# Optimization experiments

Measured on AMD Instinct MI355X. Metric: run time of the kernel, lower is better.

Reference implementation:

```python
import jax, jax.numpy as jnp
import numpy as np

B, S, DIM = 32, 1, 4096
NH, NKV, HD = 32, 8, 128
N_REP = NH // NKV
MAX_SEQ = 2048
START_POS = 2047


def setup_inputs() -> dict:
    key = jax.random.key(0)
    ks = jax.random.split(key, 10)
    t = jnp.arange(S) + START_POS  # absolute positions of the new tokens
    inv_freq = 1.0 / (10000.0 ** (jnp.arange(0, HD, 2, dtype=jnp.float32) / HD))  # [HD/2]
    angles = t[:, None].astype(jnp.float32) * inv_freq[None, :]  # [S, HD/2]
    return {
        "x": jax.random.normal(ks[0], (B, S, DIM), dtype=jnp.float32),
        "freqs_cos": jnp.cos(angles),
        "freqs_sin": jnp.sin(angles),
        "cache_k": jax.random.normal(ks[1], (B, MAX_SEQ, NKV, HD), dtype=jnp.float32),
        "cache_v": jax.random.normal(ks[2], (B, MAX_SEQ, NKV, HD), dtype=jnp.float32),
        "wq": jax.random.normal(ks[3], (NH * HD, DIM), dtype=jnp.float32) * 0.02,
        "wk": jax.random.normal(ks[4], (NKV * HD, DIM), dtype=jnp.float32) * 0.02,
        "wv": jax.random.normal(ks[5], (NKV * HD, DIM), dtype=jnp.float32) * 0.02,
        "wo": jax.random.normal(ks[6], (NH * HD, DIM), dtype=jnp.float32).T * 0.02,  # stored [out,in]=[DIM, NH*HD]
        "start_pos": START_POS,
    }


def _apply_rope(t, cos, sin):
    # t: [B, S, H, HD]; cos/sin: [S, HD/2] -> broadcast [1, S, 1, HD/2]
    tr = t.reshape(*t.shape[:-1], HD // 2, 2)
    x0, x1 = tr[..., 0], tr[..., 1]
    c = cos[None, :, None, :]
    s = sin[None, :, None, :]
    o0 = x0 * c - x1 * s
    o1 = x0 * s + x1 * c
    return jnp.stack([o0, o1], axis=-1).reshape(t.shape)


def reference(x, freqs_cos, freqs_sin, cache_k, cache_v, wq, wk, wv, wo, start_pos):
    batch, seq_len, _ = x.shape
    xq = jnp.einsum('bsd,ed->bse', x, wq).reshape(batch, seq_len, NH, HD)
    xk = jnp.einsum('bsd,ed->bse', x, wk).reshape(batch, seq_len, NKV, HD)
    xv = jnp.einsum('bsd,ed->bse', x, wv).reshape(batch, seq_len, NKV, HD)

    xq = _apply_rope(xq, freqs_cos, freqs_sin)
    xk = _apply_rope(xk, freqs_cos, freqs_sin)

    # KV-cache scatter-write, then read prefix [0, start_pos+seq_len)
    ck = jax.lax.dynamic_update_slice(cache_k, xk, (0, start_pos, 0, 0))
    cv = jax.lax.dynamic_update_slice(cache_v, xv, (0, start_pos, 0, 0))
    T = start_pos + seq_len  # static Python int
    keys = ck[:, :T]    # [B, T, NKV, HD]
    values = cv[:, :T]  # [B, T, NKV, HD]

    # GQA without materializing repeat_kv: group query heads by kv head
    q = xq.reshape(batch, seq_len, NKV, N_REP, HD)
    scores = jnp.einsum('bsgrd,btgd->bgrst', q, keys) / jnp.sqrt(jnp.float32(HD))
    probs = jax.nn.softmax(scores.astype(jnp.float32), axis=-1).astype(xq.dtype)
    out = jnp.einsum('bgrst,btgd->bsgrd', probs, values)  # [B, S, NKV, N_REP, HD]
    out = out.reshape(batch, seq_len, NH * HD)
    return jnp.einsum('bse,de->bsd', out, wo)
```

## Files before the change

kernel.cpp:

```cpp
#include <hip/hip_runtime.h>
#include <hip/hip_bf16.h>

#define B     32
#define DIM   4096
#define NH    32
#define NKV   8
#define HD    128
#define TCACHE 2048
#define NREP  4
#define SPLIT 8
#define TS    256
#define CHUNK 256
#define NCH   (DIM / CHUNK)

__device__ __forceinline__ void gemm16_core(
    const float* __restrict__ inp, const float* __restrict__ W,
    float* __restrict__ outp, int stride, int row0, bool rope,
    const float* __restrict__ fc, const float* __restrict__ fs,
    float (*xs)[B][CHUNK])
{
    const int tid = threadIdx.x;
    const int rp  = tid >> 6;
    const int kt  = tid & 63;
    const int r0  = row0 + rp * 2;

    const float* w0 = W + (size_t)r0 * DIM;
    const float* w1 = w0 + DIM;

    const int sb = tid >> 4;
    const int sc = (tid << 4) & 255;
    const float* sbase = inp + (size_t)sb * DIM + sc;

    float acc0[B], acc1[B];
#pragma unroll
    for (int b = 0; b < B; ++b) { acc0[b] = 0.f; acc1[b] = 0.f; }

    float4 xr0 = *(const float4*)(sbase);
    float4 xr1 = *(const float4*)(sbase + 4);
    float4 xr2 = *(const float4*)(sbase + 8);
    float4 xr3 = *(const float4*)(sbase + 12);
    float4 wa0 = *(const float4*)(w0 + kt * 4);
    float4 wa1 = *(const float4*)(w1 + kt * 4);
    *(float4*)(&xs[0][sb][sc])      = xr0;
    *(float4*)(&xs[0][sb][sc + 4])  = xr1;
    *(float4*)(&xs[0][sb][sc + 8])  = xr2;
    *(float4*)(&xs[0][sb][sc + 12]) = xr3;

    int buf = 0;
    for (int ch = 0; ch < NCH; ++ch) {
        __syncthreads();
        float4 wb0, wb1;
        const bool more = (ch + 1 < NCH);
        if (more) {
            const int k1 = (ch + 1) * CHUNK;
            xr0 = *(const float4*)(sbase + k1);
            xr1 = *(const float4*)(sbase + k1 + 4);
            xr2 = *(const float4*)(sbase + k1 + 8);
            xr3 = *(const float4*)(sbase + k1 + 12);
            wb0 = *(const float4*)(w0 + k1 + kt * 4);
            wb1 = *(const float4*)(w1 + k1 + kt * 4);
        }
        const float* xrow = &xs[buf][0][kt * 4];
#pragma unroll
        for (int b = 0; b < B; ++b) {
            float4 xv = *(const float4*)(xrow + b * CHUNK);
            acc0[b] = fmaf(wa0.x, xv.x, acc0[b]);
            acc0[b] = fmaf(wa0.y, xv.y, acc0[b]);
            acc0[b] = fmaf(wa0.z, xv.z, acc0[b]);
            acc0[b] = fmaf(wa0.w, xv.w, acc0[b]);
            acc1[b] = fmaf(wa1.x, xv.x, acc1[b]);
            acc1[b] = fmaf(wa1.y, xv.y, acc1[b]);
            acc1[b] = fmaf(wa1.z, xv.z, acc1[b]);
            acc1[b] = fmaf(wa1.w, xv.w, acc1[b]);
        }
        if (more) {
            *(float4*)(&xs[buf ^ 1][sb][sc])      = xr0;
            *(float4*)(&xs[buf ^ 1][sb][sc + 4])  = xr1;
            *(float4*)(&xs[buf ^ 1][sb][sc + 8])  = xr2;
            *(float4*)(&xs[buf ^ 1][sb][sc + 12]) = xr3;
            wa0 = wb0; wa1 = wb1;
        }
        buf ^= 1;
    }

#pragma unroll
    for (int b = 0; b < B; ++b) {
        float v0 = acc0[b], v1 = acc1[b];
        for (int off = 1; off < 64; off <<= 1) {
            v0 += __shfl_xor(v0, off);
            v1 += __shfl_xor(v1, off);
        }
        acc0[b] = v0; acc1[b] = v1;
    }
    if (kt == 0) {
        float c = 1.f, s = 0.f;
        if (rope) { int i = (r0 & (HD - 1)) >> 1; c = fc[i]; s = fs[i]; }
#pragma unroll
        for (int b = 0; b < B; ++b) {
            float o0 = acc0[b], o1 = acc1[b];
            if (rope) { float t0 = o0 * c - o1 * s; o1 = o0 * s + o1 * c; o0 = t0; }
            outp[(size_t)b * stride + r0]     = o0;
            outp[(size_t)b * stride + r0 + 1] = o1;
        }
    }
}

__global__ __launch_bounds__(512) void qkv_gemm(
    const float* __restrict__ x,
    const float* __restrict__ wq, const float* __restrict__ wk, const float* __restrict__ wv,
    float* __restrict__ qo, float* __restrict__ ko, float* __restrict__ vo,
    const float* __restrict__ fc, const float* __restrict__ fs)
{
    __shared__ float xs[2][B][CHUNK];
    int blk = blockIdx.x;
    const float* W; float* outp; int stride, row0; bool rope;
    if (blk < 256)      { W = wq; outp = qo; stride = NH * HD;  row0 = blk * 16;         rope = true;  }
    else if (blk < 320) { W = wk; outp = ko; stride = NKV * HD; row0 = (blk - 256) * 16; rope = true;  }
    else                { W = wv; outp = vo; stride = NKV * HD; row0 = (blk - 320) * 16; rope = false; }
    gemm16_core(x, W, outp, stride, row0, rope, fc, fs, xs);
}

__global__ __launch_bounds__(512) void gemm_wo(
    const float* __restrict__ inp, const float* __restrict__ W, float* __restrict__ outp)
{
    __shared__ float xs[2][B][CHUNK];
    gemm16_core(inp, W, outp, DIM, blockIdx.x * 16, false, nullptr, nullptr, xs);
}

__global__ __launch_bounds__(256) void attn_split_k(
    const float* __restrict__ qr, const float* __restrict__ kn, const float* __restrict__ vn,
    const float* __restrict__ ck, const float* __restrict__ cv,
    float* __restrict__ part_o, float* __restrict__ part_ml)
{
    __shared__ float q_lds[NREP][HD];
    __shared__ float p_lds[TS][NREP];
    __shared__ float red[4][NREP];
    __shared__ float o_scr[8][NREP][HD];

    const int bid = blockIdx.x;
    const int s = bid & 7, h = (bid >> 3) & 7, b = bid >> 6;
    const int t0 = s * TS;
    const int tid = threadIdx.x;

    for (int i = tid; i < NREP * HD; i += 256)
        q_lds[i >> 7][i & 127] = qr[((size_t)b * NH + h * NREP + (i >> 7)) * HD + (i & 127)];
    __syncthreads();

    const int t = t0 + tid;
    const float* kptr = (t == TCACHE - 1)
        ? (kn + ((size_t)b * NKV + h) * HD)
        : (ck + (((size_t)b * TCACHE + t) * NKV + h) * HD);
    float s0 = 0.f, s1 = 0.f, s2 = 0.f, s3 = 0.f;
#pragma unroll 8
    for (int d = 0; d < HD; d += 4) {
        float4 kv = *(const float4*)(kptr + d);
        float4 q0 = *(const float4*)(&q_lds[0][d]);
        float4 q1 = *(const float4*)(&q_lds[1][d]);
        float4 q2 = *(const float4*)(&q_lds[2][d]);
        float4 q3 = *(const float4*)(&q_lds[3][d]);
        s0 = fmaf(q0.x, kv.x, s0); s0 = fmaf(q0.y, kv.y, s0); s0 = fmaf(q0.z, kv.z, s0); s0 = fmaf(q0.w, kv.w, s0);
        s1 = fmaf(q1.x, kv.x, s1); s1 = fmaf(q1.y, kv.y, s1); s1 = fmaf(q1.z, kv.z, s1); s1 = fmaf(q1.w, kv.w, s1);
        s2 = fmaf(q2.x, kv.x, s2); s2 = fmaf(q2.y, kv.y, s2); s2 = fmaf(q2.z, kv.z, s2); s2 = fmaf(q2.w, kv.w, s2);
        s3 = fmaf(q3.x, kv.x, s3); s3 = fmaf(q3.y, kv.y, s3); s3 = fmaf(q3.z, kv.z, s3); s3 = fmaf(q3.w, kv.w, s3);
    }
    const float scale = 0.088388347648318447f;
    s0 *= scale; s1 *= scale; s2 *= scale; s3 *= scale;

    float m0 = s0, m1 = s1, m2 = s2, m3 = s3;
    for (int off = 1; off < 64; off <<= 1) {
        m0 = fmaxf(m0, __shfl_xor(m0, off));
        m1 = fmaxf(m1, __shfl_xor(m1, off));
        m2 = fmaxf(m2, __shfl_xor(m2, off));
        m3 = fmaxf(m3, __shfl_xor(m3, off));
    }
    const int wv_ = tid >> 6, lane = tid & 63;
    if (lane == 0) { red[wv_][0] = m0; red[wv_][1] = m1; red[wv_][2] = m2; red[wv_][3] = m3; }
    __syncthreads();
    m0 = fmaxf(fmaxf(red[0][0], red[1][0]), fmaxf(red[2][0], red[3][0]));
    m1 = fmaxf(fmaxf(red[0][1], red[1][1]), fmaxf(red[2][1], red[3][1]));
    m2 = fmaxf(fmaxf(red[0][2], red[1][2]), fmaxf(red[2][2], red[3][2]));
    m3 = fmaxf(fmaxf(red[0][3], red[1][3]), fmaxf(red[2][3], red[3][3]));
    float p0 = __expf(s0 - m0), p1 = __expf(s1 - m1), p2 = __expf(s2 - m2), p3 = __expf(s3 - m3);
    *(float4*)(&p_lds[tid][0]) = make_float4(p0, p1, p2, p3);
    float l0 = p0, l1 = p1, l2 = p2, l3 = p3;
    for (int off = 1; off < 64; off <<= 1) {
        l0 += __shfl_xor(l0, off);
        l1 += __shfl_xor(l1, off);
        l2 += __shfl_xor(l2, off);
        l3 += __shfl_xor(l3, off);
    }
    __syncthreads();
    if (lane == 0) { red[wv_][0] = l0; red[wv_][1] = l1; red[wv_][2] = l2; red[wv_][3] = l3; }
    __syncthreads();
    if (tid < NREP) {
        float l = red[0][tid] + red[1][tid] + red[2][tid] + red[3][tid];
        float m = (tid == 0) ? m0 : (tid == 1) ? m1 : (tid == 2) ? m2 : m3;
        part_ml[(size_t)bid * 8 + tid * 2]     = m;
        part_ml[(size_t)bid * 8 + tid * 2 + 1] = l;
    }

    const int g  = tid >> 5;
    const int dl = (tid & 31) << 2;
    float4 a0 = make_float4(0,0,0,0), a1 = a0, a2 = a0, a3 = a0;
    const int tb = t0 + g * 32;
#pragma unroll 4
    for (int j = 0; j < 32; ++j) {
        int tt = tb + j;
        const float* vptr = (tt == TCACHE - 1)
            ? (vn + ((size_t)b * NKV + h) * HD)
            : (cv + (((size_t)b * TCACHE + tt) * NKV + h) * HD);
        float4 vvv = *(const float4*)(vptr + dl);
        float4 pp  = *(const float4*)(&p_lds[g * 32 + j][0]);
        a0.x = fmaf(pp.x, vvv.x, a0.x); a0.y = fmaf(pp.x, vvv.y, a0.y); a0.z = fmaf(pp.x, vvv.z, a0.z); a0.w = fmaf(pp.x, vvv.w, a0.w);
        a1.x = fmaf(pp.y, vvv.x, a1.x); a1.y = fmaf(pp.y, vvv.y, a1.y); a1.z = fmaf(pp.y, vvv.z, a1.z); a1.w = fmaf(pp.y, vvv.w, a1.w);
        a2.x = fmaf(pp.z, vvv.x, a2.x); a2.y = fmaf(pp.z, vvv.y, a2.y); a2.z = fmaf(pp.z, vvv.z, a2.z); a2.w = fmaf(pp.z, vvv.w, a2.w);
        a3.x = fmaf(pp.w, vvv.x, a3.x); a3.y = fmaf(pp.w, vvv.y, a3.y); a3.z = fmaf(pp.w, vvv.z, a3.z); a3.w = fmaf(pp.w, vvv.w, a3.w);
    }
    *(float4*)(&o_scr[g][0][dl]) = a0;
    *(float4*)(&o_scr[g][1][dl]) = a1;
    *(float4*)(&o_scr[g][2][dl]) = a2;
    *(float4*)(&o_scr[g][3][dl]) = a3;
    __syncthreads();
    for (int oi = tid; oi < NREP * HD; oi += 256) {
        int r = oi >> 7, d = oi & 127;
        float sum = 0.f;
#pragma unroll
        for (int gg = 0; gg < 8; ++gg) sum += o_scr[gg][r][d];
        part_o[((size_t)bid * NREP + r) * HD + d] = sum;
    }
}

__global__ __launch_bounds__(128) void attn_combine(
    const float* __restrict__ part_o, const float* __restrict__ part_ml,
    float* __restrict__ attn_out)
{
    const int bh = blockIdx.x;
    const int d  = threadIdx.x;
    const int b = bh >> 3, h = bh & 7;
#pragma unroll
    for (int r = 0; r < NREP; ++r) {
        float ms[SPLIT], ls[SPLIT];
        float M = -1e30f;
#pragma unroll
        for (int s = 0; s < SPLIT; ++s) {
            ms[s] = part_ml[(size_t)(bh * SPLIT + s) * 8 + r * 2];
            ls[s] = part_ml[(size_t)(bh * SPLIT + s) * 8 + r * 2 + 1];
            M = fmaxf(M, ms[s]);
        }
        float L = 0.f, o = 0.f;
#pragma unroll
        for (int s = 0; s < SPLIT; ++s) {
            float w = __expf(ms[s] - M);
            L += ls[s] * w;
            o = fmaf(w, part_o[((size_t)(bh * SPLIT + s) * NREP + r) * HD + d], o);
        }
        attn_out[((size_t)b * NH + (h * NREP + r)) * HD + d] = o / L;
    }
}

extern "C" void kernel_launch(void* const* d_in, const int* in_sizes, int n_in,
                              void* d_out, int out_size, void* d_ws, size_t ws_size,
                              hipStream_t stream)
{
    const float* x  = (const float*)d_in[0];
    const float* fc = (const float*)d_in[1];
    const float* fs = (const float*)d_in[2];
    const float* ck = (const float*)d_in[3];
    const float* cv = (const float*)d_in[4];
    const float* wq = (const float*)d_in[5];
    const float* wk = (const float*)d_in[6];
    const float* wv = (const float*)d_in[7];
    const float* wo = (const float*)d_in[8];

    float* ws   = (float*)d_ws;
    float* q_r  = ws;
    float* k_n  = ws + 131072;
    float* v_n  = ws + 163840;
    float* a_o  = ws + 196608;
    float* p_o  = ws + 327680;
    float* p_ml = ws + 1376256;
    float* outp = (float*)d_out;

    qkv_gemm<<<dim3(384), dim3(512), 0, stream>>>(x, wq, wk, wv, q_r, k_n, v_n, fc, fs);
    attn_split_k<<<dim3(B * NKV * SPLIT), dim3(256), 0, stream>>>(q_r, k_n, v_n, ck, cv, p_o, p_ml);
    attn_combine<<<dim3(B * NKV), dim3(128), 0, stream>>>(p_o, p_ml, a_o);
    gemm_wo<<<dim3(256), dim3(512), 0, stream>>>(a_o, wo, outp);
}
```

Baseline: 214.2 us.

## Coalesce attention K/V reads and split Wo GEMM over K with atomics

The attention kernel now reads K rows cooperatively: 32 lanes each load a float4 slice of one row, and the dot products are reduced with shuffles, replacing the per-thread strided row reads. V accumulation is changed to 64-lane float2 loads per row with 4 groups. Separately, the Wo GEMM is split into two K halves across 512 blocks, and the halves are summed with atomicAdd into an output that a new kernel zeroes first. This targets uncoalesced cache reads and low Wo-GEMM occupancy, at the cost of more shuffle work, atomics, an extra launch, and float summation order that is no longer deterministic.

After: 255.3 us. 19.2% more time.

```diff
diff --git a/kernel.cpp b/kernel.cpp
--- a/kernel.cpp
+++ b/kernel.cpp
@@ -11,25 +11,24 @@
 #define SPLIT 8
 #define TS    256
 #define CHUNK 256
-#define NCH   (DIM / CHUNK)
 
 __device__ __forceinline__ void gemm16_core(
     const float* __restrict__ inp, const float* __restrict__ W,
     float* __restrict__ outp, int stride, int row0, bool rope,
     const float* __restrict__ fc, const float* __restrict__ fs,
-    float (*xs)[B][CHUNK])
+    float (*xs)[B][CHUNK], int kbeg, int nch, bool atomic)
 {
     const int tid = threadIdx.x;
     const int rp  = tid >> 6;
     const int kt  = tid & 63;
     const int r0  = row0 + rp * 2;
 
-    const float* w0 = W + (size_t)r0 * DIM;
+    const float* w0 = W + (size_t)r0 * DIM + kbeg;
     const float* w1 = w0 + DIM;
 
     const int sb = tid >> 4;
     const int sc = (tid << 4) & 255;
-    const float* sbase = inp + (size_t)sb * DIM + sc;
+    const float* sbase = inp + (size_t)sb * DIM + kbeg + sc;
 
     float acc0[B], acc1[B];
 #pragma unroll
@@ -47,10 +46,10 @@
     *(float4*)(&xs[0][sb][sc + 12]) = xr3;
 
     int buf = 0;
-    for (int ch = 0; ch < NCH; ++ch) {
+    for (int ch = 0; ch < nch; ++ch) {
         __syncthreads();
         float4 wb0, wb1;
-        const bool more = (ch + 1 < NCH);
+        const bool more = (ch + 1 < nch);
         if (more) {
             const int k1 = (ch + 1) * CHUNK;
             xr0 = *(const float4*)(sbase + k1);
@@ -99,8 +98,13 @@
         for (int b = 0; b < B; ++b) {
             float o0 = acc0[b], o1 = acc1[b];
             if (rope) { float t0 = o0 * c - o1 * s; o1 = o0 * s + o1 * c; o0 = t0; }
-            outp[(size_t)b * stride + r0]     = o0;
-            outp[(size_t)b * stride + r0 + 1] = o1;
+            if (atomic) {
+                atomicAdd(&outp[(size_t)b * stride + r0],     o0);
+                atomicAdd(&outp[(size_t)b * stride + r0 + 1], o1);
+            } else {
+                outp[(size_t)b * stride + r0]     = o0;
+                outp[(size_t)b * stride + r0 + 1] = o1;
+            }
         }
     }
 }
@@ -117,14 +121,23 @@
     if (blk < 256)      { W = wq; outp = qo; stride = NH * HD;  row0 = blk * 16;         rope = true;  }
     else if (blk < 320) { W = wk; outp = ko; stride = NKV * HD; row0 = (blk - 256) * 16; rope = true;  }
     else                { W = wv; outp = vo; stride = NKV * HD; row0 = (blk - 320) * 16; rope = false; }
-    gemm16_core(x, W, outp, stride, row0, rope, fc, fs, xs);
-}
-
-__global__ __launch_bounds__(512) void gemm_wo(
+    gemm16_core(x, W, outp, stride, row0, rope, fc, fs, xs, 0, DIM / CHUNK, false);
+}
+
+__global__ __launch_bounds__(512) void gemm_wo_split(
     const float* __restrict__ inp, const float* __restrict__ W, float* __restrict__ outp)
 {
     __shared__ float xs[2][B][CHUNK];
-    gemm16_core(inp, W, outp, DIM, blockIdx.x * 16, false, nullptr, nullptr, xs);
+    const int rowblk = blockIdx.x >> 1;
+    const int kh     = blockIdx.x & 1;
+    gemm16_core(inp, W, outp, DIM, rowblk * 16, false, nullptr, nullptr, xs,
+                kh * (DIM / 2), (DIM / 2) / CHUNK, true);
+}
+
+__global__ __launch_bounds__(256) void zero_out_kernel(float4* __restrict__ p, int n4)
+{
+    int i = blockIdx.x * 256 + threadIdx.x;
+    if (i < n4) p[i] = make_float4(0.f, 0.f, 0.f, 0.f);
 }
 
 __global__ __launch_bounds__(256) void attn_split_k(
@@ -132,36 +145,64 @@
     const float* __restrict__ ck, const float* __restrict__ cv,
     float* __restrict__ part_o, float* __restrict__ part_ml)
 {
-    __shared__ float q_lds[NREP][HD];
     __shared__ float p_lds[TS][NREP];
     __shared__ float red[4][NREP];
-    __shared__ float o_scr[8][NREP][HD];
+    __shared__ float o_scr[4][NREP][HD];
 
     const int bid = blockIdx.x;
     const int s = bid & 7, h = (bid >> 3) & 7, b = bid >> 6;
     const int t0 = s * TS;
     const int tid = threadIdx.x;
-
-    for (int i = tid; i < NREP * HD; i += 256)
-        q_lds[i >> 7][i & 127] = qr[((size_t)b * NH + h * NREP + (i >> 7)) * HD + (i & 127)];
-    __syncthreads();
-
-    const int t = t0 + tid;
-    const float* kptr = (t == TCACHE - 1)
-        ? (kn + ((size_t)b * NKV + h) * HD)
-        : (ck + (((size_t)b * TCACHE + t) * NKV + h) * HD);
+    const int l32 = tid & 31;
+    const int g   = tid >> 5;
+    const int dl  = l32 << 2;
+
+    const float* qbase = qr + ((size_t)b * NH + h * NREP) * HD + dl;
+    const float4 q0 = *(const float4*)(qbase);
+    const float4 q1 = *(const float4*)(qbase + HD);
+    const float4 q2 = *(const float4*)(qbase + 2 * HD);
+    const float4 q3 = *(const float4*)(qbase + 3 * HD);
+
+    const float* kbase = ck + (((size_t)b * TCACHE + t0) * NKV + h) * HD;
+    const float* knew  = kn + ((size_t)b * NKV + h) * HD;
+
     float s0 = 0.f, s1 = 0.f, s2 = 0.f, s3 = 0.f;
-#pragma unroll 8
-    for (int d = 0; d < HD; d += 4) {
-        float4 kv = *(const float4*)(kptr + d);
-        float4 q0 = *(const float4*)(&q_lds[0][d]);
-        float4 q1 = *(const float4*)(&q_lds[1][d]);
-        float4 q2 = *(const float4*)(&q_lds[2][d]);
-        float4 q3 = *(const float4*)(&q_lds[3][d]);
-        s0 = fmaf(q0.x, kv.x, s0); s0 = fmaf(q0.y, kv.y, s0); s0 = fmaf(q0.z, kv.z, s0); s0 = fmaf(q0.w, kv.w, s0);
-        s1 = fmaf(q1.x, kv.x, s1); s1 = fmaf(q1.y, kv.y, s1); s1 = fmaf(q1.z, kv.z, s1); s1 = fmaf(q1.w, kv.w, s1);
-        s2 = fmaf(q2.x, kv.x, s2); s2 = fmaf(q2.y, kv.y, s2); s2 = fmaf(q2.z, kv.z, s2); s2 = fmaf(q2.w, kv.w, s2);
-        s3 = fmaf(q3.x, kv.x, s3); s3 = fmaf(q3.y, kv.y, s3); s3 = fmaf(q3.z, kv.z, s3); s3 = fmaf(q3.w, kv.w, s3);
+    const int rowbase = g * 32;
+#pragma unroll
+    for (int jj = 0; jj < 8; ++jj) {
+        float4 kv[4];
+#pragma unroll
+        for (int u = 0; u < 4; ++u) {
+            const int r = rowbase + jj + 8 * u;
+            const float* kp = (t0 + r == TCACHE - 1) ? knew
+                              : (kbase + (size_t)r * (NKV * HD));
+            kv[u] = *(const float4*)(kp + dl);
+        }
+        float d_[4][NREP];
+#pragma unroll
+        for (int u = 0; u < 4; ++u) {
+            float4 k4 = kv[u];
+            float e0 = q0.x * k4.x, e1 = q1.x * k4.x, e2 = q2.x * k4.x, e3 = q3.x * k4.x;
+            e0 = fmaf(q0.y, k4.y, e0); e1 = fmaf(q1.y, k4.y, e1); e2 = fmaf(q2.y, k4.y, e2); e3 = fmaf(q3.y, k4.y, e3);
+            e0 = fmaf(q0.z, k4.z, e0); e1 = fmaf(q1.z, k4.z, e1); e2 = fmaf(q2.z, k4.z, e2); e3 = fmaf(q3.z, k4.z, e3);
+            e0 = fmaf(q0.w, k4.w, e0); e1 = fmaf(q1.w, k4.w, e1); e2 = fmaf(q2.w, k4.w, e2); e3 = fmaf(q3.w, k4.w, e3);
+            d_[u][0] = e0; d_[u][1] = e1; d_[u][2] = e2; d_[u][3] = e3;
+        }
+#pragma unroll
+        for (int off = 1; off < 32; off <<= 1) {
+#pragma unroll
+            for (int u = 0; u < 4; ++u) {
+#pragma unroll
+                for (int r = 0; r < NREP; ++r)
+                    d_[u][r] += __shfl_xor(d_[u][r], off);
+            }
+        }
+#pragma unroll
+        for (int u = 0; u < 4; ++u) {
+            if (l32 == jj + 8 * u) {
+                s0 = d_[u][0]; s1 = d_[u][1]; s2 = d_[u][2]; s3 = d_[u][3];
+            }
+        }
     }
     const float scale = 0.088388347648318447f;
     s0 *= scale; s1 *= scale; s2 *= scale; s3 *= scale;
@@ -199,33 +240,33 @@
         part_ml[(size_t)bid * 8 + tid * 2 + 1] = l;
     }
 
-    const int g  = tid >> 5;
-    const int dl = (tid & 31) << 2;
-    float4 a0 = make_float4(0,0,0,0), a1 = a0, a2 = a0, a3 = a0;
-    const int tb = t0 + g * 32;
+    const int g2   = tid >> 6;
+    const int dl2  = lane << 1;
+    const float* vbase = cv + (((size_t)b * TCACHE + t0) * NKV + h) * HD;
+    const float* vnew  = vn + ((size_t)b * NKV + h) * HD;
+    float a0x = 0.f, a0y = 0.f, a1x = 0.f, a1y = 0.f;
+    float a2x = 0.f, a2y = 0.f, a3x = 0.f, a3y = 0.f;
+    const int rb2 = g2 * 64;
 #pragma unroll 4
-    for (int j = 0; j < 32; ++j) {
-        int tt = tb + j;
-        const float* vptr = (tt == TCACHE - 1)
-            ? (vn + ((size_t)b * NKV + h) * HD)
-            : (cv + (((size_t)b * TCACHE + tt) * NKV + h) * HD);
-        float4 vvv = *(const float4*)(vptr + dl);
-        float4 pp  = *(const float4*)(&p_lds[g * 32 + j][0]);
-        a0.x = fmaf(pp.x, vvv.x, a0.x); a0.y = fmaf(pp.x, vvv.y, a0.y); a0.z = fmaf(pp.x, vvv.z, a0.z); a0.w = fmaf(pp.x, vvv.w, a0.w);
-        a1.x = fmaf(pp.y, vvv.x, a1.x); a1.y = fmaf(pp.y, vvv.y, a1.y); a1.z = fmaf(pp.y, vvv.z, a1.z); a1.w = fmaf(pp.y, vvv.w, a1.w);
-        a2.x = fmaf(pp.z, vvv.x, a2.x); a2.y = fmaf(pp.z, vvv.y, a2.y); a2.z = fmaf(pp.z, vvv.z, a2.z); a2.w = fmaf(pp.z, vvv.w, a2.w);
-        a3.x = fmaf(pp.w, vvv.x, a3.x); a3.y = fmaf(pp.w, vvv.y, a3.y); a3.z = fmaf(pp.w, vvv.z, a3.z); a3.w = fmaf(pp.w, vvv.w, a3.w);
-    }
-    *(float4*)(&o_scr[g][0][dl]) = a0;
-    *(float4*)(&o_scr[g][1][dl]) = a1;
-    *(float4*)(&o_scr[g][2][dl]) = a2;
-    *(float4*)(&o_scr[g][3][dl]) = a3;
+    for (int j = 0; j < 64; ++j) {
+        const int r = rb2 + j;
+        const float* vp = (t0 + r == TCACHE - 1) ? vnew
+                          : (vbase + (size_t)r * (NKV * HD));
+        float2 vv = *(const float2*)(vp + dl2);
+        float4 pp = *(const float4*)(&p_lds[r][0]);
+        a0x = fmaf(pp.x, vv.x, a0x); a0y = fmaf(pp.x, vv.y, a0y);
+        a1x = fmaf(pp.y, vv.x, a1x); a1y = fmaf(pp.y, vv.y, a1y);
+        a2x = fmaf(pp.z, vv.x, a2x); a2y = fmaf(pp.z, vv.y, a2y);
+        a3x = fmaf(pp.w, vv.x, a3x); a3y = fmaf(pp.w, vv.y, a3y);
+    }
+    *(float2*)(&o_scr[g2][0][dl2]) = make_float2(a0x, a0y);
+    *(float2*)(&o_scr[g2][1][dl2]) = make_float2(a1x, a1y);
+    *(float2*)(&o_scr[g2][2][dl2]) = make_float2(a2x, a2y);
+    *(float2*)(&o_scr[g2][3][dl2]) = make_float2(a3x, a3y);
     __syncthreads();
     for (int oi = tid; oi < NREP * HD; oi += 256) {
         int r = oi >> 7, d = oi & 127;
-        float sum = 0.f;
-#pragma unroll
-        for (int gg = 0; gg < 8; ++gg) sum += o_scr[gg][r][d];
+        float sum = o_scr[0][r][d] + o_scr[1][r][d] + o_scr[2][r][d] + o_scr[3][r][d];
         part_o[((size_t)bid * NREP + r) * HD + d] = sum;
     }
 }
@@ -281,8 +322,10 @@
     float* p_ml = ws + 1376256;
     float* outp = (float*)d_out;
 
+    zero_out_kernel<<<dim3((out_size / 4 + 255) / 256), dim3(256), 0, stream>>>(
+        (float4*)outp, out_size / 4);
     qkv_gemm<<<dim3(384), dim3(512), 0, stream>>>(x, wq, wk, wv, q_r, k_n, v_n, fc, fs);
     attn_split_k<<<dim3(B * NKV * SPLIT), dim3(256), 0, stream>>>(q_r, k_n, v_n, ck, cv, p_o, p_ml);
     attn_combine<<<dim3(B * NKV), dim3(128), 0, stream>>>(p_o, p_ml, a_o);
-    gemm_wo<<<dim3(256), dim3(512), 0, stream>>>(a_o, wo, outp);
-}
+    gemm_wo_split<<<dim3(512), dim3(512), 0, stream>>>(a_o, wo, outp);
+}
```
